# Kernel tuning notes

Measured on AMD Instinct MI355X. Metric: run time of the kernel, lower is better.

## Reference

```python
import jax, jax.numpy as jnp
import numpy as np

# dims: T x B x IN input, weight (H, K, IN), state (B, H, K)
T, B, IN, H, K = 512, 32, 256, 256, 10
GAP = 0.5                      # gap_penalty buffer (not trainable)
ALPHA = (1.0 / 0.5 ** 2) / K   # exp kernel: 1/sigma^2, divided by kmer_size in __init__
EPS = 1e-4


def setup_inputs() -> dict:
    key = jax.random.key(0)
    k1, k2 = jax.random.split(key)
    x = jax.random.normal(k1, (T, B, IN), dtype=jnp.float32)
    stdv = 1.0 / np.sqrt(H)    # reset_parameters: uniform(-1/sqrt(hidden), 1/sqrt(hidden))
    weight = jax.random.uniform(k2, (H, K, IN), dtype=jnp.float32, minval=-stdv, maxval=stdv)
    return {"x": x, "weight": weight}


def _kappa(u):
    # kernels['exp'](x, alpha) = exp(alpha * (x - 1))
    return jnp.exp(ALPHA * (u - 1.0))


def _matrix_inverse_sqrt(m, eps=1e-4):
    # ops.matrix_inverse_sqrt: symmetric eig, clamp eigenvalues, M^{-1/2}
    e, v = jnp.linalg.eigh(m)
    return (v * (1.0 / jnp.sqrt(jnp.clip(e, eps)))) @ v.T


def _forward(x, wn):
    # ---- _conv_layer: per-step RKHS feature map ----
    norm = jnp.linalg.norm(x, axis=-1, keepdims=True)[..., None]      # T,B,1,1
    b = jnp.einsum('tbi,hki->tbhk', x, wn)                            # T,B,H,K
    b = norm * _kappa(b / jnp.clip(norm, EPS))

    # ---- _compute_lintrans: prod over kmer of kappa(gram), then inverse sqrt ----
    gram = _kappa(jnp.einsum('hki,gki->khg', wn, wn))                 # K,H,H
    lin = _matrix_inverse_sqrt(jnp.prod(gram, axis=0))                # H,H (symmetric)

    # ---- gap-penalty recurrence over time (rkn_forward, multiplicative) ----
    # c_t[j] = gap * c_{t-1}[j] + c_{t-1}[j-1] * b_t[j],  c_{t-1}[0-1] := 1
    hx0 = jnp.zeros((B, H, K), dtype=x.dtype)
    def step(hx, bt):
        prev = jnp.concatenate([jnp.ones_like(hx[..., :1]), hx[..., :-1]], axis=-1)
        hx = GAP * hx + prev * bt
        return hx, hx
    hx_T, cs = jax.lax.scan(step, hx0, b)                             # cs: T,B,H,K

    # ---- mean pooling + select last kmer index + whitening by lintrans ----
    output = cs.mean(axis=0)[..., -1] @ lin                           # B,H (torch.mm)
    outputs = cs[..., -1] @ lin                                       # T,B,H (F.linear; lin symmetric)
    return output, outputs, hx_T


def reference(x, weight):
    # normalize_(weight, dim=-1): unit-norm each (h,k) filter over input dim
    wn = weight / jnp.clip(jnp.linalg.norm(weight, axis=-1, keepdims=True), EPS)
    return _forward(x, wn)
```

## Files before the change

kernel.cpp:

```cpp
#include <hip/hip_runtime.h>
#include <hip/hip_bf16.h>

#define T_DIM 512
#define B_DIM 32
#define IN_DIM 256
#define H_DIM 256
#define K_DIM 10
#define TB 16384
#define NKH 2560
#define NPOW 3

typedef __attribute__((ext_vector_type(8))) short short8;
typedef __attribute__((ext_vector_type(4))) float f32x4;

#define GLOBAL_AS __attribute__((address_space(1)))
#define LDS_AS __attribute__((address_space(3)))

__device__ __forceinline__ float wave_sum64(float v) {
    #pragma unroll
    for (int off = 32; off > 0; off >>= 1) v += __shfl_xor(v, off, 64);
    return v;
}

__global__ __launch_bounds__(256) void wnorm_kernel(const float* __restrict__ w,
        __hip_bfloat16* __restrict__ wb, __hip_bfloat16* __restrict__ wb2) {
    int wv = threadIdx.x >> 6, lane = threadIdx.x & 63;
    int row = blockIdx.x * 4 + wv;
    const float* src = w + (size_t)row * IN_DIM;
    float v[4]; float s = 0.f;
    #pragma unroll
    for (int j = 0; j < 4; ++j) { v[j] = src[lane + 64 * j]; s += v[j] * v[j]; }
    s = wave_sum64(s);
    float inv = 1.f / fmaxf(sqrtf(s), 1e-4f);
    int h = row / K_DIM, k = row % K_DIM;
    __hip_bfloat16* d1 = wb + (size_t)(k * H_DIM + h) * IN_DIM;
    __hip_bfloat16* d2 = wb2 + (size_t)h * NKH + k * IN_DIM;
    #pragma unroll
    for (int j = 0; j < 4; ++j) {
        __hip_bfloat16 t = __float2bfloat16(v[j] * inv);
        d1[lane + 64 * j] = t;
        d2[lane + 64 * j] = t;
    }
}

__global__ __launch_bounds__(256) void xnorm_kernel(const float* __restrict__ x,
        float* __restrict__ xninfo, __hip_bfloat16* __restrict__ xb) {
    int wv = threadIdx.x >> 6, lane = threadIdx.x & 63;
    int row = blockIdx.x * 4 + wv;
    const float* src = x + (size_t)row * IN_DIM;
    float v[4]; float s = 0.f;
    #pragma unroll
    for (int j = 0; j < 4; ++j) { v[j] = src[lane + 64 * j]; s += v[j] * v[j]; }
    s = wave_sum64(s);
    float nrm = sqrtf(s);
    if (lane == 0) { xninfo[2 * row] = nrm; xninfo[2 * row + 1] = 1.f / fmaxf(nrm, 1e-4f); }
    __hip_bfloat16* d = xb + (size_t)row * IN_DIM;
    #pragma unroll
    for (int j = 0; j < 4; ++j) d[lane + 64 * j] = __float2bfloat16(v[j]);
}

__global__ __launch_bounds__(256) void gemm_b_mfma(const __hip_bfloat16* __restrict__ xb,
        const __hip_bfloat16* __restrict__ wb, const float* __restrict__ xninfo,
        __hip_bfloat16* __restrict__ bmat) {
    __shared__ __hip_bfloat16 As[4096];
    __shared__ __hip_bfloat16 Bs[4096];
    int tid = threadIdx.x;
    int wid = tid >> 6, lane = tid & 63;
    int m0 = blockIdx.x * 128, n0 = blockIdx.y * 128;
    int wr = wid >> 1, wc = wid & 1;
    int srow = tid >> 2;
    int scol = (tid & 3) * 8;
    f32x4 acc[4][4] = {};

    for (int kb = 0; kb < IN_DIM; kb += 32) {
        #pragma unroll
        for (int half = 0; half < 2; ++half) {
            const __hip_bfloat16* ga = xb + (size_t)(m0 + half * 64 + srow) * IN_DIM + kb + scol;
            const __hip_bfloat16* gb = wb + (size_t)(n0 + half * 64 + srow) * IN_DIM + kb + scol;
            __builtin_amdgcn_global_load_lds((const GLOBAL_AS void*)ga,
                (LDS_AS void*)(As + half * 2048 + wid * 512), 16, 0, 0);
            __builtin_amdgcn_global_load_lds((const GLOBAL_AS void*)gb,
                (LDS_AS void*)(Bs + half * 2048 + wid * 512), 16, 0, 0);
        }
        __syncthreads();
        int seg = (lane >> 4) * 8;
        int rl = lane & 15;
        short8 a[4], b[4];
        #pragma unroll
        for (int m = 0; m < 4; ++m)
            a[m] = *(const short8*)(As + (wr * 64 + m * 16 + rl) * 32 + seg);
        #pragma unroll
        for (int n = 0; n < 4; ++n)
            b[n] = *(const short8*)(Bs + (wc * 64 + n * 16 + rl) * 32 + seg);
        #pragma unroll
        for (int m = 0; m < 4; ++m)
            #pragma unroll
            for (int n = 0; n < 4; ++n)
                acc[m][n] = __builtin_amdgcn_mfma_f32_16x16x32_bf16(a[m], b[n], acc[m][n], 0, 0, 0);
        __syncthreads();
    }

    int kk = blockIdx.y >> 1;
    int col_l = lane & 15;
    int rseg = (lane >> 4) * 4;
    #pragma unroll
    for (int m = 0; m < 4; ++m) {
        int rbase = m0 + wr * 64 + m * 16 + rseg;
        float4 q0 = *(const float4*)(xninfo + 2 * rbase);
        float4 q1 = *(const float4*)(xninfo + 2 * rbase + 4);
        float nrm[4] = { q0.x, q0.z, q1.x, q1.z };
        float inv[4] = { q0.y, q0.w, q1.y, q1.w };
        #pragma unroll
        for (int n = 0; n < 4; ++n) {
            int col = n0 + wc * 64 + n * 16 + col_l;
            int h = col & 255;
            #pragma unroll
            for (int j = 0; j < 4; ++j) {
                float bv = nrm[j] * __expf(0.4f * acc[m][n][j] * inv[j] - 0.4f);
                bmat[((size_t)(rbase + j) * K_DIM + kk) * H_DIM + h] = __float2bfloat16(bv);
            }
        }
    }
}

__global__ __launch_bounds__(256) void gram_partial(const __hip_bfloat16* __restrict__ wb2,
        float* __restrict__ Mpart) {
    __shared__ __hip_bfloat16 As[4096];
    __shared__ __hip_bfloat16 Bs[4096];
    int tid = threadIdx.x;
    int wid = tid >> 6, lane = tid & 63;
    int m0 = blockIdx.x * 128, n0 = blockIdx.y * 128;
    int kz = blockIdx.z;
    int wr = wid >> 1, wc = wid & 1;
    int srow = tid >> 2;
    int scol = (tid & 3) * 8;
    f32x4 acc[4][4] = {};

    for (int ks = 0; ks < 5; ++ks) {
        int kb = kz * 160 + ks * 32;
        #pragma unroll
        for (int half = 0; half < 2; ++half) {
            const __hip_bfloat16* ga = wb2 + (size_t)(m0 + half * 64 + srow) * NKH + kb + scol;
            const __hip_bfloat16* gb = wb2 + (size_t)(n0 + half * 64 + srow) * NKH + kb + scol;
            __builtin_amdgcn_global_load_lds((const GLOBAL_AS void*)ga,
                (LDS_AS void*)(As + half * 2048 + wid * 512), 16, 0, 0);
            __builtin_amdgcn_global_load_lds((const GLOBAL_AS void*)gb,
                (LDS_AS void*)(Bs + half * 2048 + wid * 512), 16, 0, 0);
        }
        __syncthreads();
        int seg = (lane >> 4) * 8;
        int rl = lane & 15;
        short8 a[4], b[4];
        #pragma unroll
        for (int m = 0; m < 4; ++m)
            a[m] = *(const short8*)(As + (wr * 64 + m * 16 + rl) * 32 + seg);
        #pragma unroll
        for (int n = 0; n < 4; ++n)
            b[n] = *(const short8*)(Bs + (wc * 64 + n * 16 + rl) * 32 + seg);
        #pragma unroll
        for (int m = 0; m < 4; ++m)
            #pragma unroll
            for (int n = 0; n < 4; ++n)
                acc[m][n] = __builtin_amdgcn_mfma_f32_16x16x32_bf16(a[m], b[n], acc[m][n], 0, 0, 0);
        __syncthreads();
    }

    float* dst = Mpart + (size_t)kz * 65536;
    int col_l = lane & 15;
    int rseg = (lane >> 4) * 4;
    #pragma unroll
    for (int m = 0; m < 4; ++m) {
        int rbase = m0 + wr * 64 + m * 16 + rseg;
        #pragma unroll
        for (int n = 0; n < 4; ++n) {
            int col = n0 + wc * 64 + n * 16 + col_l;
            #pragma unroll
            for (int j = 0; j < 4; ++j)
                dst[(size_t)(rbase + j) * H_DIM + col] = acc[m][n][j];
        }
    }
}

__global__ __launch_bounds__(256) void gram_finish(const float* __restrict__ Mpart,
        float* __restrict__ Mm, float* __restrict__ rsum) {
    __shared__ float red[256];
    int r = blockIdx.x, c = threadIdx.x;
    float s = 0.f;
    #pragma unroll
    for (int kz = 0; kz < 16; ++kz)
        s += Mpart[(size_t)kz * 65536 + (size_t)r * H_DIM + c];
    float e = __expf(0.4f * s - 4.0f);
    Mm[(size_t)r * H_DIM + c] = e;
    red[c] = e;
    __syncthreads();
    #pragma unroll
    for (int st = 128; st > 0; st >>= 1) {
        if (c < st) red[c] += red[c + st];
        __syncthreads();
    }
    if (c == 0) rsum[r] = red[0];
}

__global__ __launch_bounds__(256) void rec_kernel(const __hip_bfloat16* __restrict__ bmat,
        __hip_bfloat16* __restrict__ cs9b, float* __restrict__ part, float* __restrict__ hxT) {
    int s = blockIdx.x >> 5;
    int b = blockIdx.x & 31;
    int h = threadIdx.x;
    int tout0 = s * 64;
    int t0 = (s == 0) ? 0 : tout0 - 32;
    int t1 = tout0 + 64;
    float c[10] = {};
    float s9 = 0.f;
    float bt[10];
    {
        const __hip_bfloat16* bp = bmat + ((size_t)(t0 * B_DIM + b) * K_DIM) * H_DIM + h;
        #pragma unroll
        for (int k = 0; k < 10; ++k) bt[k] = __bfloat162float(bp[k * H_DIM]);
    }
    for (int t = t0; t < t1; ++t) {
        int tn = (t + 1 < t1) ? t + 1 : t;
        float btn[10];
        const __hip_bfloat16* bq = bmat + ((size_t)(tn * B_DIM + b) * K_DIM) * H_DIM + h;
        #pragma unroll
        for (int k = 0; k < 10; ++k) btn[k] = __bfloat162float(bq[k * H_DIM]);
        #pragma unroll
        for (int j = 9; j >= 1; --j) c[j] = 0.5f * c[j] + c[j - 1] * bt[j];
        c[0] = 0.5f * c[0] + bt[0];
        if (t >= tout0) {
            cs9b[(size_t)(t * B_DIM + b) * H_DIM + h] = __float2bfloat16(c[9]);
            s9 += c[9];
        }
        #pragma unroll
        for (int k = 0; k < 10; ++k) bt[k] = btn[k];
    }
    part[(size_t)(s * B_DIM + b) * H_DIM + h] = s9;
    if (s == 7) {
        float* hp = hxT + (size_t)(b * H_DIM + h) * K_DIM;
        #pragma unroll
        for (int k = 0; k < 10; ++k) hp[k] = c[k];
    }
}

__global__ __launch_bounds__(256) void recred_kernel(const float* __restrict__ part,
        float* __restrict__ mean9) {
    int i = blockIdx.x * 256 + threadIdx.x;
    float s = 0.f;
    #pragma unroll
    for (int j = 0; j < 8; ++j) s += part[(size_t)j * 8192 + i];
    mean9[i] = s * (1.f / T_DIM);
}

__global__ __launch_bounds__(512) void power_kernel(const float* __restrict__ Mm,
        const float* __restrict__ rsum, float* __restrict__ vbuf, float* __restrict__ cbuf) {
    __shared__ float vv[256];
    __shared__ float yv[256];
    __shared__ float red[512];
    int tid = threadIdx.x;
    if (tid < 256) vv[tid] = rsum[tid];
    __syncthreads();
    for (int it = 0; it <= NPOW; ++it) {
        int col = tid & 255, q = tid >> 8;
        const float* mp = Mm + (size_t)q * 128 * 256 + col;
        float p = 0.f;
        #pragma unroll 8
        for (int g = 0; g < 128; ++g) p = fmaf(mp[(size_t)g * 256], vv[q * 128 + g], p);
        red[tid] = p;
        __syncthreads();
        if (it < NPOW) {
            if (tid < 256) {
                float y = red[tid] + red[tid + 256];
                yv[tid] = y;
                red[tid] = y * y;
            }
            __syncthreads();
            #pragma unroll
            for (int st = 128; st > 0; st >>= 1) {
                if (tid < st) red[tid] += red[tid + st];
                __syncthreads();
            }
            float inv = rsqrtf(red[0]);
            if (tid < 256) vv[tid] = yv[tid] * inv;
            __syncthreads();
        } else {
            if (tid < 256) red[tid] = (red[tid] + red[tid + 256]) * vv[tid];
            __syncthreads();
            #pragma unroll
            for (int st = 128; st > 0; st >>= 1) {
                if (tid < st) red[tid] += red[tid + st];
                __syncthreads();
            }
            if (tid == 0) {
                float lam = red[0];
                cbuf[0] = lam;
                cbuf[1] = lam - 1.f;
                cbuf[2] = rsqrtf(lam) - 1.f;
            }
        }
    }
    if (tid < 256) vbuf[tid] = vv[tid];
}

__global__ __launch_bounds__(256) void e2_kernel(const float* __restrict__ Mm,
        const float* __restrict__ vbuf, const float* __restrict__ cbuf,
        float* __restrict__ E2g, __hip_bfloat16* __restrict__ e2b) {
    __shared__ __hip_bfloat16 EA[16384];
    __shared__ __hip_bfloat16 EC[16384];
    __shared__ float vv[256];
    int tid = threadIdx.x;
    int r0 = (blockIdx.x >> 2) * 64, c0 = (blockIdx.x & 3) * 64;
    float lm1 = cbuf[1];
    if (tid < 256) vv[tid] = vbuf[tid];
    __syncthreads();
    char* pa = (char*)EA;
    char* pc = (char*)EC;
    for (int f = tid; f < 4096; f += 256) {
        int row = f >> 6, c4 = (f & 63) << 2;
        {
            int r = r0 + row;
            float4 mv = *(const float4*)(Mm + (size_t)r * 256 + c4);
            float vr = lm1 * vv[r];
            __hip_bfloat16 hb[4];
            hb[0] = __float2bfloat16(mv.x - ((r == c4 + 0) ? 1.f : 0.f) - vr * vv[c4 + 0]);
            hb[1] = __float2bfloat16(mv.y - ((r == c4 + 1) ? 1.f : 0.f) - vr * vv[c4 + 1]);
            hb[2] = __float2bfloat16(mv.z - ((r == c4 + 2) ? 1.f : 0.f) - vr * vv[c4 + 2]);
            hb[3] = __float2bfloat16(mv.w - ((r == c4 + 3) ? 1.f : 0.f) - vr * vv[c4 + 3]);
            *(short4*)(pa + row * 512 + ((c4 * 2) ^ ((row & 7) << 4))) = *(short4*)hb;
        }
        {
            int r = c0 + row;
            float4 mv = *(const float4*)(Mm + (size_t)r * 256 + c4);
            float vr = lm1 * vv[r];
            __hip_bfloat16 hb[4];
            hb[0] = __float2bfloat16(mv.x - ((r == c4 + 0) ? 1.f : 0.f) - vr * vv[c4 + 0]);
            hb[1] = __float2bfloat16(mv.y - ((r == c4 + 1) ? 1.f : 0.f) - vr * vv[c4 + 1]);
            hb[2] = __float2bfloat16(mv.z - ((r == c4 + 2) ? 1.f : 0.f) - vr * vv[c4 + 2]);
            hb[3] = __float2bfloat16(mv.w - ((r == c4 + 3) ? 1.f : 0.f) - vr * vv[c4 + 3]);
            *(short4*)(pc + row * 512 + ((c4 * 2) ^ ((row & 7) << 4))) = *(short4*)hb;
        }
    }
    __syncthreads();
    int wv = tid >> 6, lane = tid & 63;
    int rl = lane & 15, seg8 = (lane >> 4) * 8;
    f32x4 acc[4] = {};
    for (int kb = 0; kb < 256; kb += 32) {
        int row = wv * 16 + rl;
        short8 a = *(const short8*)(pa + row * 512 + (((kb + seg8) * 2) ^ ((rl & 7) << 4)));
        short8 b[4];
        #pragma unroll
        for (int n = 0; n < 4; ++n) {
            int rowb = n * 16 + rl;
            b[n] = *(const short8*)(pc + rowb * 512 + (((kb + seg8) * 2) ^ ((rl & 7) << 4)));
        }
        #pragma unroll
        for (int n = 0; n < 4; ++n)
            acc[n] = __builtin_amdgcn_mfma_f32_16x16x32_bf16(a, b[n], acc[n], 0, 0, 0);
    }
    int col_l = lane & 15, rseg = (lane >> 4) * 4;
    #pragma unroll
    for (int n = 0; n < 4; ++n) {
        #pragma unroll
        for (int j = 0; j < 4; ++j) {
            int r = r0 + wv * 16 + rseg + j;
            int c = c0 + n * 16 + col_l;
            size_t idx = (size_t)r * 256 + c;
            E2g[idx] = acc[n][j];
            e2b[idx] = __float2bfloat16(acc[n][j]);
        }
    }
}

__global__ __launch_bounds__(256) void e3lin_kernel(const float* __restrict__ Mm,
        const float* __restrict__ vbuf, const float* __restrict__ cbuf,
        const float* __restrict__ E2g, const __hip_bfloat16* __restrict__ e2b,
        float* __restrict__ lin, __hip_bfloat16* __restrict__ linb) {
    __shared__ __hip_bfloat16 EA[16384];
    __shared__ __hip_bfloat16 EC[16384];
    __shared__ float vv[256];
    int tid = threadIdx.x;
    int r0 = (blockIdx.x >> 2) * 64, c0 = (blockIdx.x & 3) * 64;
    float lm1 = cbuf[1];
    float wfac = 0.5f * cbuf[1] + cbuf[2];
    if (tid < 256) vv[tid] = vbuf[tid];
    __syncthreads();
    char* pa = (char*)EA;
    char* pc = (char*)EC;
    for (int f = tid; f < 4096; f += 256) {
        int row = f >> 6, c4 = (f & 63) << 2;
        int r = r0 + row;
        float4 mv = *(const float4*)(Mm + (size_t)r * 256 + c4);
        float vr = lm1 * vv[r];
        __hip_bfloat16 hb[4];
        hb[0] = __float2bfloat16(mv.x - ((r == c4 + 0) ? 1.f : 0.f) - vr * vv[c4 + 0]);
        hb[1] = __float2bfloat16(mv.y - ((r == c4 + 1) ? 1.f : 0.f) - vr * vv[c4 + 1]);
        hb[2] = __float2bfloat16(mv.z - ((r == c4 + 2) ? 1.f : 0.f) - vr * vv[c4 + 2]);
        hb[3] = __float2bfloat16(mv.w - ((r == c4 + 3) ? 1.f : 0.f) - vr * vv[c4 + 3]);
        *(short4*)(pa + row * 512 + ((c4 * 2) ^ ((row & 7) << 4))) = *(short4*)hb;
    }
    for (int f = tid; f < 2048; f += 256) {
        int row = f >> 5, c8 = (f & 31) << 3;
        short8 v8 = *(const short8*)(e2b + (size_t)(c0 + row) * 256 + c8);
        *(short8*)(pc + row * 512 + ((c8 * 2) ^ ((row & 7) << 4))) = v8;
    }
    __syncthreads();
    int wv = tid >> 6, lane = tid & 63;
    int rl = lane & 15, seg8 = (lane >> 4) * 8;
    f32x4 acc[4] = {};
    for (int kb = 0; kb < 256; kb += 32) {
        int row = wv * 16 + rl;
        short8 a = *(const short8*)(pa + row * 512 + (((kb + seg8) * 2) ^ ((rl & 7) << 4)));
        short8 b[4];
        #pragma unroll
        for (int n = 0; n < 4; ++n) {
            int rowb = n * 16 + rl;
            b[n] = *(const short8*)(pc + rowb * 512 + (((kb + seg8) * 2) ^ ((rl & 7) << 4)));
        }
        #pragma unroll
        for (int n = 0; n < 4; ++n)
            acc[n] = __builtin_amdgcn_mfma_f32_16x16x32_bf16(a, b[n], acc[n], 0, 0, 0);
    }
    int col_l = lane & 15, rseg = (lane >> 4) * 4;
    #pragma unroll
    for (int n = 0; n < 4; ++n) {
        #pragma unroll
        for (int j = 0; j < 4; ++j) {
            int r = r0 + wv * 16 + rseg + j;
            int c = c0 + n * 16 + col_l;
            size_t idx = (size_t)r * 256 + c;
            float lv = ((r == c) ? 1.5f : 0.f) - 0.5f * Mm[idx] + wfac * vv[r] * vv[c]
                     + 0.375f * E2g[idx] - 0.3125f * acc[n][j];
            lin[idx] = lv;
            linb[idx] = __float2bfloat16(lv);
        }
    }
}

__global__ __launch_bounds__(256) void outmean_kernel(const float* __restrict__ mean9,
        const float* __restrict__ lin, float* __restrict__ out) {
    int b = blockIdx.x, g = threadIdx.x;
    float acc = 0.f;
    const float* mrow = mean9 + b * H_DIM;
    #pragma unroll 8
    for (int h = 0; h < H_DIM; ++h) acc = fmaf(mrow[h], lin[(size_t)h * H_DIM + g], acc);
    out[b * H_DIM + g] = acc;
}

__global__ __launch_bounds__(256) void mm_out1_mfma(const __hip_bfloat16* __restrict__ A,
        const __hip_bfloat16* __restrict__ Bt, float* __restrict__ C) {
    __shared__ __hip_bfloat16 As[4096];
    __shared__ __hip_bfloat16 Bs[4096];
    int tid = threadIdx.x;
    int wid = tid >> 6, lane = tid & 63;
    int m0 = blockIdx.x * 128, n0 = blockIdx.y * 128;
    int wr = wid >> 1, wc = wid & 1;
    int srow = tid >> 2;
    int scol = (tid & 3) * 8;
    f32x4 acc[4][4] = {};

    for (int kb = 0; kb < 256; kb += 32) {
        #pragma unroll
        for (int half = 0; half < 2; ++half) {
            const __hip_bfloat16* ga = A + (size_t)(m0 + half * 64 + srow) * 256 + kb + scol;
            const __hip_bfloat16* gb = Bt + (size_t)(n0 + half * 64 + srow) * 256 + kb + scol;
            __builtin_amdgcn_global_load_lds((const GLOBAL_AS void*)ga,
                (LDS_AS void*)(As + half * 2048 + wid * 512), 16, 0, 0);
            __builtin_amdgcn_global_load_lds((const GLOBAL_AS void*)gb,
                (LDS_AS void*)(Bs + half * 2048 + wid * 512), 16, 0, 0);
        }
        __syncthreads();
        int seg = (lane >> 4) * 8;
        int rl = lane & 15;
        short8 a[4], b[4];
        #pragma unroll
        for (int m = 0; m < 4; ++m)
            a[m] = *(const short8*)(As + (wr * 64 + m * 16 + rl) * 32 + seg);
        #pragma unroll
        for (int n = 0; n < 4; ++n)
            b[n] = *(const short8*)(Bs + (wc * 64 + n * 16 + rl) * 32 + seg);
        #pragma unroll
        for (int m = 0; m < 4; ++m)
            #pragma unroll
            for (int n = 0; n < 4; ++n)
                acc[m][n] = __builtin_amdgcn_mfma_f32_16x16x32_bf16(a[m], b[n], acc[m][n], 0, 0, 0);
        __syncthreads();
    }

    int col_l = lane & 15;
    int rseg = (lane >> 4) * 4;
    #pragma unroll
    for (int m = 0; m < 4; ++m) {
        int rbase = m0 + wr * 64 + m * 16 + rseg;
        #pragma unroll
        for (int n = 0; n < 4; ++n) {
            int col = n0 + wc * 64 + n * 16 + col_l;
            #pragma unroll
            for (int j = 0; j < 4; ++j)
                C[(size_t)(rbase + j) * 256 + col] = acc[m][n][j];
        }
    }
}

extern "C" void kernel_launch(void* const* d_in, const int* in_sizes, int n_in,
                              void* d_out, int out_size, void* d_ws, size_t ws_size,
                              hipStream_t stream) {
    const float* x = (const float*)d_in[0];
    const float* w = (const float*)d_in[1];
    float* out0 = (float*)d_out;
    float* out1 = out0 + (size_t)B_DIM * H_DIM;
    float* hxT  = out1 + (size_t)TB * H_DIM;

    char* ws = (char*)d_ws;
    __hip_bfloat16* wb   = (__hip_bfloat16*)(ws + 0);
    __hip_bfloat16* wb2  = (__hip_bfloat16*)(ws + 1310720);
    float* xninfo        = (float*)(ws + 2621440);
    float* Mm            = (float*)(ws + 2752512);
    float* rsum          = (float*)(ws + 3014656);
    float* E2g           = (float*)(ws + 3015680);
    __hip_bfloat16* e2b  = (__hip_bfloat16*)(ws + 3277824);
    float* lin           = (float*)(ws + 3408896);
    __hip_bfloat16* linb = (__hip_bfloat16*)(ws + 3671040);
    float* vbuf          = (float*)(ws + 3802112);
    float* cbuf          = (float*)(ws + 3803136);
    float* mean9         = (float*)(ws + 3804160);
    float* part          = (float*)(ws + 3836928);
    __hip_bfloat16* cs9b = (__hip_bfloat16*)(ws + 4099072);
    float* Mpart         = (float*)cs9b;
    __hip_bfloat16* xb   = (__hip_bfloat16*)(ws + 12487680);
    __hip_bfloat16* bmat = (__hip_bfloat16*)(ws + 20876288);

    wnorm_kernel<<<dim3(640), dim3(256), 0, stream>>>(w, wb, wb2);
    xnorm_kernel<<<dim3(4096), dim3(256), 0, stream>>>(x, xninfo, xb);
    gram_partial<<<dim3(2, 2, 16), dim3(256), 0, stream>>>(wb2, Mpart);
    gram_finish<<<dim3(256), dim3(256), 0, stream>>>(Mpart, Mm, rsum);
    power_kernel<<<dim3(1), dim3(512), 0, stream>>>(Mm, rsum, vbuf, cbuf);
    e2_kernel<<<dim3(16), dim3(256), 0, stream>>>(Mm, vbuf, cbuf, E2g, e2b);
    e3lin_kernel<<<dim3(16), dim3(256), 0, stream>>>(Mm, vbuf, cbuf, E2g, e2b, lin, linb);
    gemm_b_mfma<<<dim3(128, 20), dim3(256), 0, stream>>>(xb, wb, xninfo, bmat);
    rec_kernel<<<dim3(256), dim3(256), 0, stream>>>(bmat, cs9b, part, hxT);
    recred_kernel<<<dim3(32), dim3(256), 0, stream>>>(part, mean9);
    outmean_kernel<<<dim3(32), dim3(256), 0, stream>>>(mean9, lin, out0);
    mm_out1_mfma<<<dim3(128, 2), dim3(256), 0, stream>>>(cs9b, linb, out1);
}
```

Baseline: 156.8 us.

## Fuse recurrence with output projection and merge small kernels to cut launches

```diff
diff --git a/kernel.cpp b/kernel.cpp
--- a/kernel.cpp
+++ b/kernel.cpp
@@ -22,41 +22,41 @@
     return v;
 }
 
-__global__ __launch_bounds__(256) void wnorm_kernel(const float* __restrict__ w,
-        __hip_bfloat16* __restrict__ wb, __hip_bfloat16* __restrict__ wb2) {
+__global__ __launch_bounds__(256) void prep_kernel(const float* __restrict__ w,
+        const float* __restrict__ x, __hip_bfloat16* __restrict__ wb,
+        __hip_bfloat16* __restrict__ wb2, float* __restrict__ xninfo,
+        __hip_bfloat16* __restrict__ xb) {
     int wv = threadIdx.x >> 6, lane = threadIdx.x & 63;
-    int row = blockIdx.x * 4 + wv;
-    const float* src = w + (size_t)row * IN_DIM;
-    float v[4]; float s = 0.f;
-    #pragma unroll
-    for (int j = 0; j < 4; ++j) { v[j] = src[lane + 64 * j]; s += v[j] * v[j]; }
-    s = wave_sum64(s);
-    float inv = 1.f / fmaxf(sqrtf(s), 1e-4f);
-    int h = row / K_DIM, k = row % K_DIM;
-    __hip_bfloat16* d1 = wb + (size_t)(k * H_DIM + h) * IN_DIM;
-    __hip_bfloat16* d2 = wb2 + (size_t)h * NKH + k * IN_DIM;
-    #pragma unroll
-    for (int j = 0; j < 4; ++j) {
-        __hip_bfloat16 t = __float2bfloat16(v[j] * inv);
-        d1[lane + 64 * j] = t;
-        d2[lane + 64 * j] = t;
-    }
-}
-
-__global__ __launch_bounds__(256) void xnorm_kernel(const float* __restrict__ x,
-        float* __restrict__ xninfo, __hip_bfloat16* __restrict__ xb) {
-    int wv = threadIdx.x >> 6, lane = threadIdx.x & 63;
-    int row = blockIdx.x * 4 + wv;
-    const float* src = x + (size_t)row * IN_DIM;
-    float v[4]; float s = 0.f;
-    #pragma unroll
-    for (int j = 0; j < 4; ++j) { v[j] = src[lane + 64 * j]; s += v[j] * v[j]; }
-    s = wave_sum64(s);
-    float nrm = sqrtf(s);
-    if (lane == 0) { xninfo[2 * row] = nrm; xninfo[2 * row + 1] = 1.f / fmaxf(nrm, 1e-4f); }
-    __hip_bfloat16* d = xb + (size_t)row * IN_DIM;
-    #pragma unroll
-    for (int j = 0; j < 4; ++j) d[lane + 64 * j] = __float2bfloat16(v[j]);
+    if (blockIdx.x < 640) {
+        int row = blockIdx.x * 4 + wv;
+        const float* src = w + (size_t)row * IN_DIM;
+        float v[4]; float s = 0.f;
+        #pragma unroll
+        for (int j = 0; j < 4; ++j) { v[j] = src[lane + 64 * j]; s += v[j] * v[j]; }
+        s = wave_sum64(s);
+        float inv = 1.f / fmaxf(sqrtf(s), 1e-4f);
+        int h = row / K_DIM, k = row % K_DIM;
+        __hip_bfloat16* d1 = wb + (size_t)(k * H_DIM + h) * IN_DIM;
+        __hip_bfloat16* d2 = wb2 + (size_t)h * NKH + k * IN_DIM;
+        #pragma unroll
+        for (int j = 0; j < 4; ++j) {
+            __hip_bfloat16 t = __float2bfloat16(v[j] * inv);
+            d1[lane + 64 * j] = t;
+            d2[lane + 64 * j] = t;
+        }
+    } else {
+        int row = (blockIdx.x - 640) * 4 + wv;
+        const float* src = x + (size_t)row * IN_DIM;
+        float v[4]; float s = 0.f;
+        #pragma unroll
+        for (int j = 0; j < 4; ++j) { v[j] = src[lane + 64 * j]; s += v[j] * v[j]; }
+        s = wave_sum64(s);
+        float nrm = sqrtf(s);
+        if (lane == 0) { xninfo[2 * row] = nrm; xninfo[2 * row + 1] = 1.f / fmaxf(nrm, 1e-4f); }
+        __hip_bfloat16* d = xb + (size_t)row * IN_DIM;
+        #pragma unroll
+        for (int j = 0; j < 4; ++j) d[lane + 64 * j] = __float2bfloat16(v[j]);
+    }
 }
 
 __global__ __launch_bounds__(256) void gemm_b_mfma(const __hip_bfloat16* __restrict__ xb,
@@ -201,77 +201,18 @@
     if (c == 0) rsum[r] = red[0];
 }
 
-__global__ __launch_bounds__(256) void rec_kernel(const __hip_bfloat16* __restrict__ bmat,
-        __hip_bfloat16* __restrict__ cs9b, float* __restrict__ part, float* __restrict__ hxT) {
-    int s = blockIdx.x >> 5;
-    int b = blockIdx.x & 31;
-    int h = threadIdx.x;
-    int tout0 = s * 64;
-    int t0 = (s == 0) ? 0 : tout0 - 32;
-    int t1 = tout0 + 64;
-    float c[10] = {};
-    float s9 = 0.f;
-    float bt[10];
-    {
-        const __hip_bfloat16* bp = bmat + ((size_t)(t0 * B_DIM + b) * K_DIM) * H_DIM + h;
-        #pragma unroll
-        for (int k = 0; k < 10; ++k) bt[k] = __bfloat162float(bp[k * H_DIM]);
-    }
-    for (int t = t0; t < t1; ++t) {
-        int tn = (t + 1 < t1) ? t + 1 : t;
-        float btn[10];
-        const __hip_bfloat16* bq = bmat + ((size_t)(tn * B_DIM + b) * K_DIM) * H_DIM + h;
-        #pragma unroll
-        for (int k = 0; k < 10; ++k) btn[k] = __bfloat162float(bq[k * H_DIM]);
-        #pragma unroll
-        for (int j = 9; j >= 1; --j) c[j] = 0.5f * c[j] + c[j - 1] * bt[j];
-        c[0] = 0.5f * c[0] + bt[0];
-        if (t >= tout0) {
-            cs9b[(size_t)(t * B_DIM + b) * H_DIM + h] = __float2bfloat16(c[9]);
-            s9 += c[9];
-        }
-        #pragma unroll
-        for (int k = 0; k < 10; ++k) bt[k] = btn[k];
-    }
-    part[(size_t)(s * B_DIM + b) * H_DIM + h] = s9;
-    if (s == 7) {
-        float* hp = hxT + (size_t)(b * H_DIM + h) * K_DIM;
-        #pragma unroll
-        for (int k = 0; k < 10; ++k) hp[k] = c[k];
-    }
-}
-
-__global__ __launch_bounds__(256) void recred_kernel(const float* __restrict__ part,
-        float* __restrict__ mean9) {
-    int i = blockIdx.x * 256 + threadIdx.x;
-    float s = 0.f;
-    #pragma unroll
-    for (int j = 0; j < 8; ++j) s += part[(size_t)j * 8192 + i];
-    mean9[i] = s * (1.f / T_DIM);
-}
-
-__global__ __launch_bounds__(512) void power_kernel(const float* __restrict__ Mm,
-        const float* __restrict__ rsum, float* __restrict__ vbuf, float* __restrict__ cbuf) {
-    __shared__ float vv[256];
-    __shared__ float yv[256];
-    __shared__ float red[512];
-    int tid = threadIdx.x;
-    if (tid < 256) vv[tid] = rsum[tid];
+__device__ __forceinline__ float power_phase(const float* __restrict__ Mm,
+        const float* __restrict__ rsum, float* vv, float* red, int tid) {
+    vv[tid] = rsum[tid];
     __syncthreads();
+    float lam = 0.f;
     for (int it = 0; it <= NPOW; ++it) {
-        int col = tid & 255, q = tid >> 8;
-        const float* mp = Mm + (size_t)q * 128 * 256 + col;
         float p = 0.f;
         #pragma unroll 8
-        for (int g = 0; g < 128; ++g) p = fmaf(mp[(size_t)g * 256], vv[q * 128 + g], p);
-        red[tid] = p;
+        for (int g = 0; g < 256; ++g) p = fmaf(Mm[(size_t)g * 256 + tid], vv[g], p);
         __syncthreads();
         if (it < NPOW) {
-            if (tid < 256) {
-                float y = red[tid] + red[tid + 256];
-                yv[tid] = y;
-                red[tid] = y * y;
-            }
+            red[tid] = p * p;
             __syncthreads();
             #pragma unroll
             for (int st = 128; st > 0; st >>= 1) {
@@ -279,38 +220,35 @@
                 __syncthreads();
             }
             float inv = rsqrtf(red[0]);
-            if (tid < 256) vv[tid] = yv[tid] * inv;
+            __syncthreads();
+            vv[tid] = p * inv;
             __syncthreads();
         } else {
-            if (tid < 256) red[tid] = (red[tid] + red[tid + 256]) * vv[tid];
+            red[tid] = p * vv[tid];
             __syncthreads();
             #pragma unroll
             for (int st = 128; st > 0; st >>= 1) {
                 if (tid < st) red[tid] += red[tid + st];
                 __syncthreads();
             }
-            if (tid == 0) {
-                float lam = red[0];
-                cbuf[0] = lam;
-                cbuf[1] = lam - 1.f;
-                cbuf[2] = rsqrtf(lam) - 1.f;
-            }
-        }
-    }
-    if (tid < 256) vbuf[tid] = vv[tid];
+            lam = red[0];
+            __syncthreads();
+        }
+    }
+    return lam;
 }
 
 __global__ __launch_bounds__(256) void e2_kernel(const float* __restrict__ Mm,
-        const float* __restrict__ vbuf, const float* __restrict__ cbuf,
-        float* __restrict__ E2g, __hip_bfloat16* __restrict__ e2b) {
+        const float* __restrict__ rsum, float* __restrict__ E2g,
+        __hip_bfloat16* __restrict__ e2b) {
     __shared__ __hip_bfloat16 EA[16384];
     __shared__ __hip_bfloat16 EC[16384];
     __shared__ float vv[256];
+    __shared__ float redl[256];
     int tid = threadIdx.x;
     int r0 = (blockIdx.x >> 2) * 64, c0 = (blockIdx.x & 3) * 64;
-    float lm1 = cbuf[1];
-    if (tid < 256) vv[tid] = vbuf[tid];
-    __syncthreads();
+    float lam = power_phase(Mm, rsum, vv, redl, tid);
+    float lm1 = lam - 1.f;
     char* pa = (char*)EA;
     char* pc = (char*)EC;
     for (int f = tid; f < 4096; f += 256) {
@@ -370,18 +308,18 @@
 }
 
 __global__ __launch_bounds__(256) void e3lin_kernel(const float* __restrict__ Mm,
-        const float* __restrict__ vbuf, const float* __restrict__ cbuf,
-        const float* __restrict__ E2g, const __hip_bfloat16* __restrict__ e2b,
+        const float* __restrict__ rsum, const float* __restrict__ E2g,
+        const __hip_bfloat16* __restrict__ e2b,
         float* __restrict__ lin, __hip_bfloat16* __restrict__ linb) {
     __shared__ __hip_bfloat16 EA[16384];
     __shared__ __hip_bfloat16 EC[16384];
     __shared__ float vv[256];
+    __shared__ float redl[256];
     int tid = threadIdx.x;
     int r0 = (blockIdx.x >> 2) * 64, c0 = (blockIdx.x & 3) * 64;
-    float lm1 = cbuf[1];
-    float wfac = 0.5f * cbuf[1] + cbuf[2];
-    if (tid < 256) vv[tid] = vbuf[tid];
-    __syncthreads();
+    float lam = power_phase(Mm, rsum, vv, redl, tid);
+    float lm1 = lam - 1.f;
+    float wfac = 0.5f * lm1 + (rsqrtf(lam) - 1.f);
     char* pa = (char*)EA;
     char* pc = (char*)EC;
     for (int f = tid; f < 4096; f += 256) {
@@ -434,69 +372,98 @@
     }
 }
 
-__global__ __launch_bounds__(256) void outmean_kernel(const float* __restrict__ mean9,
-        const float* __restrict__ lin, float* __restrict__ out) {
-    int b = blockIdx.x, g = threadIdx.x;
+__global__ __launch_bounds__(256) void megarec(const __hip_bfloat16* __restrict__ bmat,
+        const __hip_bfloat16* __restrict__ linb, float* __restrict__ out1,
+        float* __restrict__ part, float* __restrict__ hxT) {
+    __shared__ __hip_bfloat16 c9t[16384];
+    int tid = threadIdx.x;
+    int s = blockIdx.x >> 5;
+    int b = blockIdx.x & 31;
+    int h = tid;
+    int tout0 = s * 64;
+    int t0 = (s == 0) ? 0 : tout0 - 32;
+    int t1 = tout0 + 64;
+    char* c9p = (char*)c9t;
+    float c[10] = {};
+    float s9 = 0.f;
+    float bt[10];
+    {
+        const __hip_bfloat16* bp = bmat + ((size_t)(t0 * B_DIM + b) * K_DIM) * H_DIM + h;
+        #pragma unroll
+        for (int k = 0; k < 10; ++k) bt[k] = __bfloat162float(bp[k * H_DIM]);
+    }
+    for (int t = t0; t < t1; ++t) {
+        int tn = (t + 1 < t1) ? t + 1 : t;
+        float btn[10];
+        const __hip_bfloat16* bq = bmat + ((size_t)(tn * B_DIM + b) * K_DIM) * H_DIM + h;
+        #pragma unroll
+        for (int k = 0; k < 10; ++k) btn[k] = __bfloat162float(bq[k * H_DIM]);
+        #pragma unroll
+        for (int j = 9; j >= 1; --j) c[j] = 0.5f * c[j] + c[j - 1] * bt[j];
+        c[0] = 0.5f * c[0] + bt[0];
+        if (t >= tout0) {
+            int tt = t - tout0;
+            *(__hip_bfloat16*)(c9p + tt * 512 + ((h * 2) ^ ((tt & 7) << 4))) = __float2bfloat16(c[9]);
+            s9 += c[9];
+        }
+        #pragma unroll
+        for (int k = 0; k < 10; ++k) bt[k] = btn[k];
+    }
+    part[(size_t)(s * B_DIM + b) * H_DIM + h] = s9;
+    if (s == 7) {
+        float* hp = hxT + (size_t)(b * H_DIM + h) * K_DIM;
+        #pragma unroll
+        for (int k = 0; k < 10; ++k) hp[k] = c[k];
+    }
+    __syncthreads();
+    int wid = tid >> 6, lane = tid & 63;
+    int rl = lane & 15, seg8 = (lane >> 4) * 8;
+    int col_l = lane & 15, rseg = (lane >> 4) * 4;
+    f32x4 acc[4][4] = {};
+    for (int kb = 0; kb < 256; kb += 32) {
+        short8 a[4];
+        #pragma unroll
+        for (int m = 0; m < 4; ++m) {
+            int row = m * 16 + rl;
+            a[m] = *(const short8*)(c9p + row * 512 + (((kb + seg8) * 2) ^ ((row & 7) << 4)));
+        }
+        short8 bf[4];
+        #pragma unroll
+        for (int n = 0; n < 4; ++n)
+            bf[n] = *(const short8*)(linb + (size_t)(wid * 64 + n * 16 + rl) * 256 + kb + seg8);
+        #pragma unroll
+        for (int m = 0; m < 4; ++m)
+            #pragma unroll
+            for (int n = 0; n < 4; ++n)
+                acc[m][n] = __builtin_amdgcn_mfma_f32_16x16x32_bf16(a[m], bf[n], acc[m][n], 0, 0, 0);
+    }
+    #pragma unroll
+    for (int m = 0; m < 4; ++m) {
+        #pragma unroll
+        for (int n = 0; n < 4; ++n) {
+            int g = wid * 64 + n * 16 + col_l;
+            #pragma unroll
+            for (int j = 0; j < 4; ++j) {
+                int tt = m * 16 + rseg + j;
+                out1[((size_t)(tout0 + tt) * B_DIM + b) * H_DIM + g] = acc[m][n][j];
+            }
+        }
+    }
+}
+
+__global__ __launch_bounds__(256) void recout_kernel(const float* __restrict__ part,
+        const float* __restrict__ lin, float* __restrict__ out0) {
+    __shared__ float mrow[256];
+    int b = blockIdx.x, tid = threadIdx.x;
+    float s = 0.f;
+    #pragma unroll
+    for (int j = 0; j < 8; ++j) s += part[(size_t)(j * B_DIM + b) * H_DIM + tid];
+    mrow[tid] = s * (1.f / T_DIM);
+    __syncthreads();
     float acc = 0.f;
-    const float* mrow = mean9 + b * H_DIM;
     #pragma unroll 8
-    for (int h = 0; h < H_DIM; ++h) acc = fmaf(mrow[h], lin[(size_t)h * H_DIM + g], acc);
-    out[b * H_DIM + g] = acc;
-}
-
-__global__ __launch_bounds__(256) void mm_out1_mfma(const __hip_bfloat16* __restrict__ A,
-        const __hip_bfloat16* __restrict__ Bt, float* __restrict__ C) {
-    __shared__ __hip_bfloat16 As[4096];
-    __shared__ __hip_bfloat16 Bs[4096];
-    int tid = threadIdx.x;
-    int wid = tid >> 6, lane = tid & 63;
-    int m0 = blockIdx.x * 128, n0 = blockIdx.y * 128;
-    int wr = wid >> 1, wc = wid & 1;
-    int srow = tid >> 2;
-    int scol = (tid & 3) * 8;
-    f32x4 acc[4][4] = {};
-
-    for (int kb = 0; kb < 256; kb += 32) {
-        #pragma unroll
-        for (int half = 0; half < 2; ++half) {
-            const __hip_bfloat16* ga = A + (size_t)(m0 + half * 64 + srow) * 256 + kb + scol;
-            const __hip_bfloat16* gb = Bt + (size_t)(n0 + half * 64 + srow) * 256 + kb + scol;
-            __builtin_amdgcn_global_load_lds((const GLOBAL_AS void*)ga,
-                (LDS_AS void*)(As + half * 2048 + wid * 512), 16, 0, 0);
-            __builtin_amdgcn_global_load_lds((const GLOBAL_AS void*)gb,
-                (LDS_AS void*)(Bs + half * 2048 + wid * 512), 16, 0, 0);
-        }
-        __syncthreads();
-        int seg = (lane >> 4) * 8;
-        int rl = lane & 15;
-        short8 a[4], b[4];
-        #pragma unroll
-        for (int m = 0; m < 4; ++m)
-            a[m] = *(const short8*)(As + (wr * 64 + m * 16 + rl) * 32 + seg);
-        #pragma unroll
-        for (int n = 0; n < 4; ++n)
-            b[n] = *(const short8*)(Bs + (wc * 64 + n * 16 + rl) * 32 + seg);
-        #pragma unroll
-        for (int m = 0; m < 4; ++m)
-            #pragma unroll
-            for (int n = 0; n < 4; ++n)
-                acc[m][n] = __builtin_amdgcn_mfma_f32_16x16x32_bf16(a[m], b[n], acc[m][n], 0, 0, 0);
-        __syncthreads();
-    }
-
-    int col_l = lane & 15;
-    int rseg = (lane >> 4) * 4;
-    #pragma unroll
-    for (int m = 0; m < 4; ++m) {
-        int rbase = m0 + wr * 64 + m * 16 + rseg;
-        #pragma unroll
-        for (int n = 0; n < 4; ++n) {
-            int col = n0 + wc * 64 + n * 16 + col_l;
-            #pragma unroll
-            for (int j = 0; j < 4; ++j)
-                C[(size_t)(rbase + j) * 256 + col] = acc[m][n][j];
-        }
-    }
+    for (int h = 0; h < H_DIM; ++h) acc = fmaf(mrow[h], lin[(size_t)h * H_DIM + tid], acc);
+    out0[b * H_DIM + tid] = acc;
 }
 
 extern "C" void kernel_launch(void* const* d_in, const int* in_sizes, int n_in,
@@ -518,25 +485,17 @@
     __hip_bfloat16* e2b  = (__hip_bfloat16*)(ws + 3277824);
     float* lin           = (float*)(ws + 3408896);
     __hip_bfloat16* linb = (__hip_bfloat16*)(ws + 3671040);
-    float* vbuf          = (float*)(ws + 3802112);
-    float* cbuf          = (float*)(ws + 3803136);
-    float* mean9         = (float*)(ws + 3804160);
-    float* part          = (float*)(ws + 3836928);
-    __hip_bfloat16* cs9b = (__hip_bfloat16*)(ws + 4099072);
-    float* Mpart         = (float*)cs9b;
-    __hip_bfloat16* xb   = (__hip_bfloat16*)(ws + 12487680);
-    __hip_bfloat16* bmat = (__hip_bfloat16*)(ws + 20876288);
-
-    wnorm_kernel<<<dim3(640), dim3(256), 0, stream>>>(w, wb, wb2);
-    xnorm_kernel<<<dim3(4096), dim3(256), 0, stream>>>(x, xninfo, xb);
+    float* part          = (float*)(ws + 3802112);
+    float* Mpart         = (float*)(ws + 4064256);
+    __hip_bfloat16* xb   = (__hip_bfloat16*)(ws + 8258560);
+    __hip_bfloat16* bmat = (__hip_bfloat16*)(ws + 16647168);
+
+    prep_kernel<<<dim3(4736), dim3(256), 0, stream>>>(w, x, wb, wb2, xninfo, xb);
+    gemm_b_mfma<<<dim3(128, 20), dim3(256), 0, stream>>>(xb, wb, xninfo, bmat);
     gram_partial<<<dim3(2, 2, 16), dim3(256), 0, stream>>>(wb2, Mpart);
     gram_finish<<<dim3(256), dim3(256), 0, stream>>>(Mpart, Mm, rsum);
-    power_kernel<<<dim3(1), dim3(512), 0, stream>>>(Mm, rsum, vbuf, cbuf);
-    e2_kernel<<<dim3(16), dim3(256), 0, stream>>>(Mm, vbuf, cbuf, E2g, e2b);
-    e3lin_kernel<<<dim3(16), dim3(256), 0, stream>>>(Mm, vbuf, cbuf, E2g, e2b, lin, linb);
-    gemm_b_mfma<<<dim3(128, 20), dim3(256), 0, stream>>>(xb, wb, xninfo, bmat);
-    rec_kernel<<<dim3(256), dim3(256), 0, stream>>>(bmat, cs9b, part, hxT);
-    recred_kernel<<<dim3(32), dim3(256), 0, stream>>>(part, mean9);
-    outmean_kernel<<<dim3(32), dim3(256), 0, stream>>>(mean9, lin, out0);
-    mm_out1_mfma<<<dim3(128, 2), dim3(256), 0, stream>>>(cs9b, linb, out1);
-}
+    e2_kernel<<<dim3(16), dim3(256), 0, stream>>>(Mm, rsum, E2g, e2b);
+    e3lin_kernel<<<dim3(16), dim3(256), 0, stream>>>(Mm, rsum, E2g, e2b, lin, linb);
+    megarec<<<dim3(256), dim3(256), 0, stream>>>(bmat, linb, out1, part, hxT);
+    recout_kernel<<<dim3(32), dim3(256), 0, stream>>>(part, lin, out0);
+}
```

New measurement: 173.8 us. +10.8%, slower.
